# Optimization experiments

Measured on AMD Instinct MI355X. Metric: run time of the kernel, lower is better.

Reference implementation:

```python
import jax, jax.numpy as jnp
import numpy as np

B = 16384
N_NEIGH = 50
D = 64
NUM_USERS = 100000
NUM_ITEMS = 100000
NUM_ENTITIES = 200000


def setup_inputs() -> dict:
    key = jax.random.key(0)
    ks = jax.random.split(key, 16)
    s = 1.0 / np.sqrt(D)
    return {
        "user_indices": jax.random.randint(ks[0], (B,), 0, NUM_USERS),
        "item_indices": jax.random.randint(ks[1], (B,), 0, NUM_ITEMS),
        "kg_adj_batch": jax.random.randint(ks[2], (B, N_NEIGH), 0, NUM_ENTITIES),
        "user_table": jax.random.normal(ks[3], (NUM_USERS, D), jnp.float32),
        "item_table": jax.random.normal(ks[4], (NUM_ITEMS, D), jnp.float32),
        "entity_table": jax.random.normal(ks[5], (NUM_ENTITIES, D), jnp.float32),
        "attn_W": jax.random.normal(ks[6], (2 * D, 1), jnp.float32) * s,
        "attn_b": jnp.zeros((1,), jnp.float32),
        "kg_W1": jax.random.normal(ks[7], (D, D), jnp.float32) * s,
        "kg_b1": jnp.zeros((D,), jnp.float32),
        "kg_W2": jax.random.normal(ks[8], (D, D), jnp.float32) * s,
        "kg_b2": jnp.zeros((D,), jnp.float32),
        "comb_W": jax.random.normal(ks[9], (2 * D, D), jnp.float32) * s,
        "comb_b": jnp.zeros((D,), jnp.float32),
        "out_W": jax.random.normal(ks[10], (2 * D, 1), jnp.float32) * s,
        "out_b": jnp.zeros((1,), jnp.float32),
    }


def reference(user_indices, item_indices, kg_adj_batch,
              user_table, item_table, entity_table,
              attn_W, attn_b, kg_W1, kg_b1, kg_W2, kg_b2,
              comb_W, comb_b, out_W, out_b):
    user_emb = user_table[user_indices]          # [B, D]
    item_emb = item_table[item_indices]          # [B, D]
    nbr_idx = jnp.clip(kg_adj_batch, 0)
    neighbor_emb = entity_table[nbr_idx]         # [B, N, D]
    # attention_linear(cat([item, nbr])) == item @ Wi + nbr @ Wn + b (avoids [B,N,2D])
    Wi, Wn = attn_W[:D], attn_W[D:]
    attn_scores = item_emb @ Wi + jnp.einsum('bnd,do->bno', neighbor_emb, Wn)[..., 0] + attn_b  # [B, N]
    attn_scores = jax.nn.leaky_relu(attn_scores, negative_slope=0.2)
    attn_weights = jax.nn.softmax(attn_scores, axis=1)                 # softmax over neighbors
    neighbor_attn = jnp.einsum('bn,bnd->bd', attn_weights, neighbor_emb)
    refined_kg = jax.nn.relu(neighbor_attn @ kg_W1 + kg_b1) @ kg_W2 + kg_b2
    combined_item = jnp.concatenate([item_emb, refined_kg], axis=1)
    final_item_rep = jax.nn.relu(combined_item @ comb_W + comb_b)      # dropout = identity (eval)
    combined_user_item = jnp.concatenate([user_emb, final_item_rep], axis=1)
    score = (combined_user_item @ out_W + out_b)[:, 0]
    return score
```

## Files before the change

### kernel.cpp

```cpp
#include <hip/hip_runtime.h>

#define NN 50
#define D 64
#define GRP 10

typedef unsigned int uint32;
typedef unsigned short ushort16;

__device__ __forceinline__ float wave_sum64(float x) {
#pragma unroll
  for (int off = 32; off > 0; off >>= 1)
    x += __shfl_xor(x, off, 64);
  return x;
}

__device__ __forceinline__ float readlane_f(float v, int l) {
  return __uint_as_float(__builtin_amdgcn_readlane(__float_as_uint(v), l));
}

__device__ __forceinline__ ushort16 f32_to_bf16(float f) {
  uint32 u = __float_as_uint(f);
  u += 0x7FFF + ((u >> 16) & 1);
  return (ushort16)(u >> 16);
}

__global__ __launch_bounds__(256, 4) void kgat_prep(
    const float* __restrict__ ent_tab, const float* __restrict__ attn_W,
    float* __restrict__ proj, ushort16* __restrict__ ent_bf, int rows,
    int pblocks,
    const float* __restrict__ W2, const float* __restrict__ b2,
    const float* __restrict__ cW, const float* __restrict__ cb,
    float* __restrict__ W2cW, float* __restrict__ cb2)
{
  const int lane = threadIdx.x & 63;
  const int wv   = threadIdx.x >> 6;

  if ((int)blockIdx.x < pblocks) {
    const long wave = (long)blockIdx.x * 4 + wv;
    const long base = wave * GRP;
    if (base >= rows) return;
    const float Wn = attn_W[D + lane];
    float v[GRP];
#pragma unroll
    for (int i = 0; i < GRP; ++i) {
      long r = base + i; if (r > rows - 1) r = rows - 1;
      v[i] = ent_tab[r * D + lane];
    }
    float s[GRP];
#pragma unroll
    for (int i = 0; i < GRP; ++i)
      s[i] = wave_sum64(v[i] * Wn);
#pragma unroll
    for (int i = 0; i < GRP; ++i) {
      const long r = base + i;
      if (r < rows) ent_bf[r * D + lane] = f32_to_bf16(v[i]);
    }
    if (lane == 0) {
#pragma unroll
      for (int i = 0; i < GRP; ++i)
        if (base + i < rows) proj[base + i] = s[i];
    }
  } else {
    const int d = ((int)blockIdx.x - pblocks) * 4 + wv;
    float acc = 0.f;
#pragma unroll 8
    for (int k = 0; k < D; ++k)
      acc = fmaf(W2[d * D + k], cW[(D + k) * D + lane], acc);
    W2cW[d * D + lane] = acc;
    if (d == 0) {
      float a2 = 0.f;
#pragma unroll 8
      for (int k = 0; k < D; ++k)
        a2 = fmaf(b2[k], cW[(D + k) * D + lane], a2);
      cb2[lane] = cb[lane] + a2;
    }
  }
}

#define PGRP 5

__device__ __forceinline__ void load_pair_grp(uint32 (&buf)[PGRP],
                                              const int* __restrict__ adjb,
                                              const uint32* __restrict__ ent32,
                                              int g, int half, int sub) {
#pragma unroll
  for (int i = 0; i < PGRP; ++i) {
    const int p = g * PGRP + i;
    int t0 = adjb[2 * p + 0]; t0 = t0 < 0 ? 0 : t0;
    int t1 = adjb[2 * p + 1]; t1 = t1 < 0 ? 0 : t1;
    const int t = half ? t1 : t0;
    buf[i] = ent32[(size_t)t * 32 + sub];
  }
}

__device__ __forceinline__ void acc_pair_grp(const uint32 (&buf)[PGRP],
                                             float e, int g, int half,
                                             float& lo0, float& lo1,
                                             float& hi0, float& hi1) {
#pragma unroll
  for (int i = 0; i < PGRP; ++i) {
    const int p = g * PGRP + i;
    const float w0 = readlane_f(e, 2 * p + 0);
    const float w1 = readlane_f(e, 2 * p + 1);
    const float w  = half ? w1 : w0;
    const float lo = __uint_as_float(buf[i] << 16);
    const float hi = __uint_as_float(buf[i] & 0xFFFF0000u);
    if (i & 1) { lo1 = fmaf(w, lo, lo1); hi1 = fmaf(w, hi, hi1); }
    else       { lo0 = fmaf(w, lo, lo0); hi0 = fmaf(w, hi, hi0); }
  }
}

__global__ __launch_bounds__(256, 4) void kgat_attn2(
    const int* __restrict__ item_idx, const int* __restrict__ adj,
    const float* __restrict__ item_tab,
    const uint32* __restrict__ ent32, const float* __restrict__ proj,
    const float* __restrict__ attn_W, const float* __restrict__ attn_b,
    float* __restrict__ naws, int B)
{
  const int lane = threadIdx.x & 63;
  const int wv   = threadIdx.x >> 6;
  const int b    = blockIdx.x * 4 + wv;
  if (b >= B) return;
  const int half = lane >> 5;
  const int sub  = lane & 31;

  const int* adjb = adj + (long)b * NN;

  uint32 GA[PGRP], GB[PGRP];
  load_pair_grp(GA, adjb, ent32, 0, half, sub);
  load_pair_grp(GB, adjb, ent32, 1, half, sub);

  const float item = item_tab[(long)item_idx[b] * D + lane];
  const float base = wave_sum64(item * attn_W[lane]) + attn_b[0];

  const int myn = lane < NN ? lane : NN - 1;
  int mi = adjb[myn]; mi = mi < 0 ? 0 : mi;
  float s = proj[mi] + base;
  s = s > 0.f ? s : 0.2f * s;
  const float e = (lane < NN) ? __expf(s - 8.0f) : 0.f;
  const float denom = wave_sum64(e);

  float lo0 = 0.f, lo1 = 0.f, hi0 = 0.f, hi1 = 0.f;
  acc_pair_grp(GA, e, 0, half, lo0, lo1, hi0, hi1);
  load_pair_grp(GA, adjb, ent32, 2, half, sub);
  acc_pair_grp(GB, e, 1, half, lo0, lo1, hi0, hi1);
  load_pair_grp(GB, adjb, ent32, 3, half, sub);
  acc_pair_grp(GA, e, 2, half, lo0, lo1, hi0, hi1);
  load_pair_grp(GA, adjb, ent32, 4, half, sub);
  acc_pair_grp(GB, e, 3, half, lo0, lo1, hi0, hi1);
  acc_pair_grp(GA, e, 4, half, lo0, lo1, hi0, hi1);

  float nlo = lo0 + lo1;
  float nhi = hi0 + hi1;
  nlo += __shfl_xor(nlo, 32, 64);
  nhi += __shfl_xor(nhi, 32, 64);

  const float inv = 1.0f / denom;
  if (lane < 32) {
    float2 val = make_float2(nlo * inv, nhi * inv);
    *(float2*)(naws + (long)b * D + 2 * sub) = val;
  }
}

__global__ __launch_bounds__(256, 4) void kgat_mlpf(
    const int* __restrict__ user_idx, const int* __restrict__ item_idx,
    const float* __restrict__ user_tab, const float* __restrict__ item_tab,
    const float* __restrict__ naws,
    const float* __restrict__ W1, const float* __restrict__ b1,
    const float* __restrict__ cW,
    const float* __restrict__ W2cW, const float* __restrict__ cb2,
    const float* __restrict__ oW, const float* __restrict__ ob,
    float* __restrict__ out, int B)
{
  __shared__ __align__(16) float s_h[4 * 4 * D];

  const int lane = threadIdx.x & 63;
  const int wv   = threadIdx.x >> 6;
  const int b0   = (blockIdx.x * 4 + wv) * 4;
  if (b0 >= B) return;

  float* shA = s_h + (wv * 4 + 0) * D;
  float* shB = s_h + (wv * 4 + 1) * D;
  float* shC = s_h + (wv * 4 + 2) * D;
  float* shD = s_h + (wv * 4 + 3) * D;

  const int bA = b0 + 0 < B ? b0 + 0 : B - 1;
  const int bB = b0 + 1 < B ? b0 + 1 : B - 1;
  const int bC = b0 + 2 < B ? b0 + 2 : B - 1;
  const int bD = b0 + 3 < B ? b0 + 3 : B - 1;

  const int uA = __builtin_amdgcn_readfirstlane(bA);
  const int uB = __builtin_amdgcn_readfirstlane(bB);
  const int uC = __builtin_amdgcn_readfirstlane(bC);
  const int uD = __builtin_amdgcn_readfirstlane(bD);
  const float* napA = naws + (long)uA * D;
  const float* napB = naws + (long)uB * D;
  const float* napC = naws + (long)uC * D;
  const float* napD = naws + (long)uD * D;
  const int iiA = __builtin_amdgcn_readfirstlane(item_idx[bA]);
  const int iiB = __builtin_amdgcn_readfirstlane(item_idx[bB]);
  const int iiC = __builtin_amdgcn_readfirstlane(item_idx[bC]);
  const int iiD = __builtin_amdgcn_readfirstlane(item_idx[bD]);
  const float* itpA = item_tab + (long)iiA * D;
  const float* itpB = item_tab + (long)iiB * D;
  const float* itpC = item_tab + (long)iiC * D;
  const float* itpD = item_tab + (long)iiD * D;

  const float usA = user_tab[(long)user_idx[bA] * D + lane];
  const float usB = user_tab[(long)user_idx[bB] * D + lane];
  const float usC = user_tab[(long)user_idx[bC] * D + lane];
  const float usD = user_tab[(long)user_idx[bD] * D + lane];

  const float b1v  = b1[lane];
  const float cb2v = cb2[lane];
  float hA0 = b1v, hA1 = 0.f, hB0 = b1v, hB1 = 0.f;
  float hC0 = b1v, hC1 = 0.f, hD0 = b1v, hD1 = 0.f;
  float fA0 = cb2v, fA1 = 0.f, fB0 = cb2v, fB1 = 0.f;
  float fC0 = cb2v, fC1 = 0.f, fD0 = cb2v, fD1 = 0.f;
#pragma unroll
  for (int d = 0; d < D; d += 4) {
    const float v0 = W1[(d + 0) * D + lane];
    const float v1 = W1[(d + 1) * D + lane];
    const float v2 = W1[(d + 2) * D + lane];
    const float v3 = W1[(d + 3) * D + lane];
    const float w0 = cW[(d + 0) * D + lane];
    const float w1 = cW[(d + 1) * D + lane];
    const float w2 = cW[(d + 2) * D + lane];
    const float w3 = cW[(d + 3) * D + lane];
    const float4 aA = *(const float4*)(napA + d);
    const float4 aB = *(const float4*)(napB + d);
    const float4 aC = *(const float4*)(napC + d);
    const float4 aD = *(const float4*)(napD + d);
    const float4 iA = *(const float4*)(itpA + d);
    const float4 iB = *(const float4*)(itpB + d);
    const float4 iC = *(const float4*)(itpC + d);
    const float4 iD = *(const float4*)(itpD + d);
    hA0 = fmaf(aA.x, v0, hA0); hA1 = fmaf(aA.y, v1, hA1);
    hA0 = fmaf(aA.z, v2, hA0); hA1 = fmaf(aA.w, v3, hA1);
    hB0 = fmaf(aB.x, v0, hB0); hB1 = fmaf(aB.y, v1, hB1);
    hB0 = fmaf(aB.z, v2, hB0); hB1 = fmaf(aB.w, v3, hB1);
    hC0 = fmaf(aC.x, v0, hC0); hC1 = fmaf(aC.y, v1, hC1);
    hC0 = fmaf(aC.z, v2, hC0); hC1 = fmaf(aC.w, v3, hC1);
    hD0 = fmaf(aD.x, v0, hD0); hD1 = fmaf(aD.y, v1, hD1);
    hD0 = fmaf(aD.z, v2, hD0); hD1 = fmaf(aD.w, v3, hD1);
    fA0 = fmaf(iA.x, w0, fA0); fA1 = fmaf(iA.y, w1, fA1);
    fA0 = fmaf(iA.z, w2, fA0); fA1 = fmaf(iA.w, w3, fA1);
    fB0 = fmaf(iB.x, w0, fB0); fB1 = fmaf(iB.y, w1, fB1);
    fB0 = fmaf(iB.z, w2, fB0); fB1 = fmaf(iB.w, w3, fB1);
    fC0 = fmaf(iC.x, w0, fC0); fC1 = fmaf(iC.y, w1, fC1);
    fC0 = fmaf(iC.z, w2, fC0); fC1 = fmaf(iC.w, w3, fC1);
    fD0 = fmaf(iD.x, w0, fD0); fD1 = fmaf(iD.y, w1, fD1);
    fD0 = fmaf(iD.z, w2, fD0); fD1 = fmaf(iD.w, w3, fD1);
  }
  shA[lane] = fmaxf(hA0 + hA1, 0.f);
  shB[lane] = fmaxf(hB0 + hB1, 0.f);
  shC[lane] = fmaxf(hC0 + hC1, 0.f);
  shD[lane] = fmaxf(hD0 + hD1, 0.f);

#pragma unroll
  for (int d = 0; d < D; d += 4) {
    const float w0 = W2cW[(d + 0) * D + lane];
    const float w1 = W2cW[(d + 1) * D + lane];
    const float w2 = W2cW[(d + 2) * D + lane];
    const float w3 = W2cW[(d + 3) * D + lane];
    const float4 cA = *(const float4*)(shA + d);
    const float4 cB = *(const float4*)(shB + d);
    const float4 cC = *(const float4*)(shC + d);
    const float4 cD = *(const float4*)(shD + d);
    fA0 = fmaf(cA.x, w0, fA0); fA1 = fmaf(cA.y, w1, fA1);
    fA0 = fmaf(cA.z, w2, fA0); fA1 = fmaf(cA.w, w3, fA1);
    fB0 = fmaf(cB.x, w0, fB0); fB1 = fmaf(cB.y, w1, fB1);
    fB0 = fmaf(cB.z, w2, fB0); fB1 = fmaf(cB.w, w3, fB1);
    fC0 = fmaf(cC.x, w0, fC0); fC1 = fmaf(cC.y, w1, fC1);
    fC0 = fmaf(cC.z, w2, fC0); fC1 = fmaf(cC.w, w3, fC1);
    fD0 = fmaf(cD.x, w0, fD0); fD1 = fmaf(cD.y, w1, fD1);
    fD0 = fmaf(cD.z, w2, fD0); fD1 = fmaf(cD.w, w3, fD1);
  }
  const float fA = fmaxf(fA0 + fA1, 0.f);
  const float fB = fmaxf(fB0 + fB1, 0.f);
  const float fC = fmaxf(fC0 + fC1, 0.f);
  const float fD = fmaxf(fD0 + fD1, 0.f);

  const float oWu = oW[lane];
  const float oWf = oW[D + lane];
  const float ob0 = ob[0];
  const float scA = wave_sum64(fmaf(usA, oWu, fA * oWf));
  const float scB = wave_sum64(fmaf(usB, oWu, fB * oWf));
  const float scC = wave_sum64(fmaf(usC, oWu, fC * oWf));
  const float scD = wave_sum64(fmaf(usD, oWu, fD * oWf));
  if (lane == 0) {
    out[bA] = scA + ob0;
    if (bB != bA) out[bB] = scB + ob0;
    if (bC != bB) out[bC] = scC + ob0;
    if (bD != bC) out[bD] = scD + ob0;
  }
}

__device__ __forceinline__ void load_grp(float (&buf)[GRP],
                                         const int* __restrict__ adjb,
                                         const float* __restrict__ ent_tab,
                                         int g, int lane) {
#pragma unroll
  for (int i = 0; i < GRP; ++i) {
    int t = adjb[g * GRP + i];
    t = t < 0 ? 0 : t;
    buf[i] = ent_tab[(long)t * D + lane];
  }
}

__device__ __forceinline__ void proc_grp(const float (&buf)[GRP],
                                         float Wn, float base,
                                         float& l0, float& l1, float& na) {
  float ex[GRP];
#pragma unroll
  for (int i = 0; i < GRP; ++i) {
    float t = wave_sum64(buf[i] * Wn) + base;
    t = t > 0.f ? t : 0.2f * t;
    ex[i] = __expf(t - 8.0f);
  }
#pragma unroll
  for (int i = 0; i < GRP; ++i) {
    if (i & 1) l1 += ex[i]; else l0 += ex[i];
    na = fmaf(ex[i], buf[i], na);
  }
}

__global__ __launch_bounds__(256, 4) void kgat_r3(
    const int* __restrict__ user_idx, const int* __restrict__ item_idx,
    const int* __restrict__ adj,
    const float* __restrict__ user_tab, const float* __restrict__ item_tab,
    const float* __restrict__ ent_tab,
    const float* __restrict__ attn_W, const float* __restrict__ attn_b,
    const float* __restrict__ W1, const float* __restrict__ b1,
    const float* __restrict__ W2, const float* __restrict__ b2,
    const float* __restrict__ cW, const float* __restrict__ cb,
    const float* __restrict__ oW, const float* __restrict__ ob,
    float* __restrict__ out, int B)
{
  const int lane = threadIdx.x & 63;
  const int wv   = threadIdx.x >> 6;
  const int b    = blockIdx.x * 4 + wv;
  if (b >= B) return;

  const float user = user_tab[(long)user_idx[b] * D + lane];
  const float oWu  = oW[lane];
  const float oWf  = oW[D + lane];
  const float item = item_tab[(long)item_idx[b] * D + lane];
  const float Wi   = attn_W[lane];
  const float Wn   = attn_W[D + lane];
  const float base = wave_sum64(item * Wi) + attn_b[0];
  const int* adjb = adj + b * NN;

  float na = 0.f, l0 = 0.f, l1 = 0.f;
  float A[GRP], Bv[GRP];
  load_grp(A,  adjb, ent_tab, 0, lane);
  load_grp(Bv, adjb, ent_tab, 1, lane);
  proc_grp(A,  Wn, base, l0, l1, na);
  load_grp(A,  adjb, ent_tab, 2, lane);
  proc_grp(Bv, Wn, base, l0, l1, na);
  load_grp(Bv, adjb, ent_tab, 3, lane);
  proc_grp(A,  Wn, base, l0, l1, na);
  load_grp(A,  adjb, ent_tab, 4, lane);
  proc_grp(Bv, Wn, base, l0, l1, na);
  proc_grp(A,  Wn, base, l0, l1, na);
  na /= (l0 + l1);

  float h0 = b1[lane], h1 = 0.f, h2 = 0.f, h3 = 0.f;
#pragma unroll
  for (int d = 0; d < D; d += 4) {
    h0 = fmaf(readlane_f(na, d + 0), W1[(d + 0) * D + lane], h0);
    h1 = fmaf(readlane_f(na, d + 1), W1[(d + 1) * D + lane], h1);
    h2 = fmaf(readlane_f(na, d + 2), W1[(d + 2) * D + lane], h2);
    h3 = fmaf(readlane_f(na, d + 3), W1[(d + 3) * D + lane], h3);
  }
  const float h = fmaxf((h0 + h1) + (h2 + h3), 0.f);

  float r0 = b2[lane], r1 = 0.f, r2 = 0.f, r3 = 0.f;
#pragma unroll
  for (int d = 0; d < D; d += 4) {
    r0 = fmaf(readlane_f(h, d + 0), W2[(d + 0) * D + lane], r0);
    r1 = fmaf(readlane_f(h, d + 1), W2[(d + 1) * D + lane], r1);
    r2 = fmaf(readlane_f(h, d + 2), W2[(d + 2) * D + lane], r2);
    r3 = fmaf(readlane_f(h, d + 3), W2[(d + 3) * D + lane], r3);
  }
  const float r = (r0 + r1) + (r2 + r3);

  float f0 = cb[lane], f1 = 0.f, f2 = 0.f, f3 = 0.f;
#pragma unroll
  for (int k = 0; k < D; k += 4) {
    f0 = fmaf(readlane_f(item, k + 0), cW[(k + 0) * D + lane], f0);
    f1 = fmaf(readlane_f(item, k + 1), cW[(k + 1) * D + lane], f1);
    f2 = fmaf(readlane_f(item, k + 2), cW[(k + 2) * D + lane], f2);
    f3 = fmaf(readlane_f(item, k + 3), cW[(k + 3) * D + lane], f3);
  }
#pragma unroll
  for (int k = 0; k < D; k += 4) {
    f0 = fmaf(readlane_f(r, k + 0), cW[(D + k + 0) * D + lane], f0);
    f1 = fmaf(readlane_f(r, k + 1), cW[(D + k + 1) * D + lane], f1);
    f2 = fmaf(readlane_f(r, k + 2), cW[(D + k + 2) * D + lane], f2);
    f3 = fmaf(readlane_f(r, k + 3), cW[(D + k + 3) * D + lane], f3);
  }
  const float f = fmaxf((f0 + f1) + (f2 + f3), 0.f);

  const float sc = wave_sum64(fmaf(user, oWu, f * oWf));
  if (lane == 0) out[b] = sc + ob[0];
}

extern "C" void kernel_launch(void* const* d_in, const int* in_sizes, int n_in,
                              void* d_out, int out_size, void* d_ws, size_t ws_size,
                              hipStream_t stream) {
  const int*   user_idx = (const int*)d_in[0];
  const int*   item_idx = (const int*)d_in[1];
  const int*   adj      = (const int*)d_in[2];
  const float* user_tab = (const float*)d_in[3];
  const float* item_tab = (const float*)d_in[4];
  const float* ent_tab  = (const float*)d_in[5];
  const float* attn_W   = (const float*)d_in[6];
  const float* attn_b   = (const float*)d_in[7];
  const float* W1       = (const float*)d_in[8];
  const float* b1       = (const float*)d_in[9];
  const float* W2       = (const float*)d_in[10];
  const float* b2       = (const float*)d_in[11];
  const float* cW       = (const float*)d_in[12];
  const float* cb       = (const float*)d_in[13];
  const float* oW       = (const float*)d_in[14];
  const float* ob       = (const float*)d_in[15];
  float* out = (float*)d_out;

  const int B    = in_sizes[0];
  const int rows = in_sizes[5] / D;

  const size_t off_bf = ((size_t)rows * 4 + 255) & ~(size_t)255;
  const size_t off_na = (off_bf + (size_t)rows * D * 2 + 255) & ~(size_t)255;
  const size_t off_w2 = (off_na + (size_t)B * D * 4 + 255) & ~(size_t)255;
  const size_t off_cb = off_w2 + (size_t)D * D * 4;
  const size_t need   = off_cb + (size_t)D * 4;

  if (ws_size >= need) {
    float*    proj   = (float*)d_ws;
    ushort16* ent_bf = (ushort16*)((char*)d_ws + off_bf);
    float*    naws   = (float*)((char*)d_ws + off_na);
    float*    W2cW   = (float*)((char*)d_ws + off_w2);
    float*    cb2    = (float*)((char*)d_ws + off_cb);
    const int waves   = (rows + GRP - 1) / GRP;
    const int pblocks = (waves + 3) / 4;
    const int ablocks = (B + 3) / 4;
    const int mblocks = (B + 15) / 16;
    kgat_prep<<<pblocks + 16, 256, 0, stream>>>(ent_tab, attn_W, proj, ent_bf,
                                                rows, pblocks, W2, b2, cW, cb,
                                                W2cW, cb2);
    kgat_attn2<<<ablocks, 256, 0, stream>>>(item_idx, adj, item_tab,
                                            (const uint32*)ent_bf, proj,
                                            attn_W, attn_b, naws, B);
    kgat_mlpf<<<mblocks, 256, 0, stream>>>(user_idx, item_idx, user_tab,
                                           item_tab, naws, W1, b1, cW,
                                           W2cW, cb2, oW, ob, out, B);
  } else {
    const int blocks = (B + 3) / 4;
    kgat_r3<<<blocks, 256, 0, stream>>>(user_idx, item_idx, adj,
                                        user_tab, item_tab, ent_tab,
                                        attn_W, attn_b, W1, b1, W2, b2,
                                        cW, cb, oW, ob, out, B);
  }
}
```

Before: 51.74 us.

## Move first KG MLP layer into attention kernel and fuse second-stage matmuls

```diff
diff --git a/kernel.cpp b/kernel.cpp
--- a/kernel.cpp
+++ b/kernel.cpp
@@ -110,12 +110,13 @@
   }
 }
 
-__global__ __launch_bounds__(256, 4) void kgat_attn2(
+__global__ __launch_bounds__(256, 4) void kgat_attn2h(
     const int* __restrict__ item_idx, const int* __restrict__ adj,
     const float* __restrict__ item_tab,
     const uint32* __restrict__ ent32, const float* __restrict__ proj,
     const float* __restrict__ attn_W, const float* __restrict__ attn_b,
-    float* __restrict__ naws, int B)
+    const float* __restrict__ W1, const float* __restrict__ b1,
+    float* __restrict__ hws, int B)
 {
   const int lane = threadIdx.x & 63;
   const int wv   = threadIdx.x >> 6;
@@ -154,36 +155,34 @@
   float nhi = hi0 + hi1;
   nlo += __shfl_xor(nlo, 32, 64);
   nhi += __shfl_xor(nhi, 32, 64);
-
   const float inv = 1.0f / denom;
-  if (lane < 32) {
-    float2 val = make_float2(nlo * inv, nhi * inv);
-    *(float2*)(naws + (long)b * D + 2 * sub) = val;
-  }
-}
-
-__global__ __launch_bounds__(256, 4) void kgat_mlpf(
+
+  float h0 = 0.f, h1 = 0.f;
+#pragma unroll
+  for (int k = 0; k < D; k += 2) {
+    const float a0 = readlane_f(nlo, k >> 1);
+    const float a1 = readlane_f(nhi, k >> 1);
+    h0 = fmaf(a0, W1[(k + 0) * D + lane], h0);
+    h1 = fmaf(a1, W1[(k + 1) * D + lane], h1);
+  }
+  const float h = fmaxf(fmaf(h0 + h1, inv, b1[lane]), 0.f);
+  hws[(long)b * D + lane] = h;
+}
+
+__global__ __launch_bounds__(256, 4) void kgat_mlp2u(
     const int* __restrict__ user_idx, const int* __restrict__ item_idx,
     const float* __restrict__ user_tab, const float* __restrict__ item_tab,
-    const float* __restrict__ naws,
-    const float* __restrict__ W1, const float* __restrict__ b1,
+    const float* __restrict__ hws,
     const float* __restrict__ cW,
     const float* __restrict__ W2cW, const float* __restrict__ cb2,
     const float* __restrict__ oW, const float* __restrict__ ob,
     float* __restrict__ out, int B)
 {
-  __shared__ __align__(16) float s_h[4 * 4 * D];
-
   const int lane = threadIdx.x & 63;
   const int wv   = threadIdx.x >> 6;
   const int b0   = (blockIdx.x * 4 + wv) * 4;
   if (b0 >= B) return;
 
-  float* shA = s_h + (wv * 4 + 0) * D;
-  float* shB = s_h + (wv * 4 + 1) * D;
-  float* shC = s_h + (wv * 4 + 2) * D;
-  float* shD = s_h + (wv * 4 + 3) * D;
-
   const int bA = b0 + 0 < B ? b0 + 0 : B - 1;
   const int bB = b0 + 1 < B ? b0 + 1 : B - 1;
   const int bC = b0 + 2 < B ? b0 + 2 : B - 1;
@@ -193,10 +192,10 @@
   const int uB = __builtin_amdgcn_readfirstlane(bB);
   const int uC = __builtin_amdgcn_readfirstlane(bC);
   const int uD = __builtin_amdgcn_readfirstlane(bD);
-  const float* napA = naws + (long)uA * D;
-  const float* napB = naws + (long)uB * D;
-  const float* napC = naws + (long)uC * D;
-  const float* napD = naws + (long)uD * D;
+  const float* hpA = hws + (long)uA * D;
+  const float* hpB = hws + (long)uB * D;
+  const float* hpC = hws + (long)uC * D;
+  const float* hpD = hws + (long)uD * D;
   const int iiA = __builtin_amdgcn_readfirstlane(item_idx[bA]);
   const int iiB = __builtin_amdgcn_readfirstlane(item_idx[bB]);
   const int iiC = __builtin_amdgcn_readfirstlane(item_idx[bC]);
@@ -211,70 +210,43 @@
   const float usC = user_tab[(long)user_idx[bC] * D + lane];
   const float usD = user_tab[(long)user_idx[bD] * D + lane];
 
-  const float b1v  = b1[lane];
   const float cb2v = cb2[lane];
-  float hA0 = b1v, hA1 = 0.f, hB0 = b1v, hB1 = 0.f;
-  float hC0 = b1v, hC1 = 0.f, hD0 = b1v, hD1 = 0.f;
   float fA0 = cb2v, fA1 = 0.f, fB0 = cb2v, fB1 = 0.f;
   float fC0 = cb2v, fC1 = 0.f, fD0 = cb2v, fD1 = 0.f;
 #pragma unroll
   for (int d = 0; d < D; d += 4) {
-    const float v0 = W1[(d + 0) * D + lane];
-    const float v1 = W1[(d + 1) * D + lane];
-    const float v2 = W1[(d + 2) * D + lane];
-    const float v3 = W1[(d + 3) * D + lane];
     const float w0 = cW[(d + 0) * D + lane];
     const float w1 = cW[(d + 1) * D + lane];
     const float w2 = cW[(d + 2) * D + lane];
     const float w3 = cW[(d + 3) * D + lane];
-    const float4 aA = *(const float4*)(napA + d);
-    const float4 aB = *(const float4*)(napB + d);
-    const float4 aC = *(const float4*)(napC + d);
-    const float4 aD = *(const float4*)(napD + d);
+    const float v0 = W2cW[(d + 0) * D + lane];
+    const float v1 = W2cW[(d + 1) * D + lane];
+    const float v2 = W2cW[(d + 2) * D + lane];
+    const float v3 = W2cW[(d + 3) * D + lane];
     const float4 iA = *(const float4*)(itpA + d);
     const float4 iB = *(const float4*)(itpB + d);
     const float4 iC = *(const float4*)(itpC + d);
     const float4 iD = *(const float4*)(itpD + d);
-    hA0 = fmaf(aA.x, v0, hA0); hA1 = fmaf(aA.y, v1, hA1);
-    hA0 = fmaf(aA.z, v2, hA0); hA1 = fmaf(aA.w, v3, hA1);
-    hB0 = fmaf(aB.x, v0, hB0); hB1 = fmaf(aB.y, v1, hB1);
-    hB0 = fmaf(aB.z, v2, hB0); hB1 = fmaf(aB.w, v3, hB1);
-    hC0 = fmaf(aC.x, v0, hC0); hC1 = fmaf(aC.y, v1, hC1);
-    hC0 = fmaf(aC.z, v2, hC0); hC1 = fmaf(aC.w, v3, hC1);
-    hD0 = fmaf(aD.x, v0, hD0); hD1 = fmaf(aD.y, v1, hD1);
-    hD0 = fmaf(aD.z, v2, hD0); hD1 = fmaf(aD.w, v3, hD1);
+    const float4 hA = *(const float4*)(hpA + d);
+    const float4 hB = *(const float4*)(hpB + d);
+    const float4 hC = *(const float4*)(hpC + d);
+    const float4 hD = *(const float4*)(hpD + d);
     fA0 = fmaf(iA.x, w0, fA0); fA1 = fmaf(iA.y, w1, fA1);
     fA0 = fmaf(iA.z, w2, fA0); fA1 = fmaf(iA.w, w3, fA1);
+    fA0 = fmaf(hA.x, v0, fA0); fA1 = fmaf(hA.y, v1, fA1);
+    fA0 = fmaf(hA.z, v2, fA0); fA1 = fmaf(hA.w, v3, fA1);
     fB0 = fmaf(iB.x, w0, fB0); fB1 = fmaf(iB.y, w1, fB1);
     fB0 = fmaf(iB.z, w2, fB0); fB1 = fmaf(iB.w, w3, fB1);
+    fB0 = fmaf(hB.x, v0, fB0); fB1 = fmaf(hB.y, v1, fB1);
+    fB0 = fmaf(hB.z, v2, fB0); fB1 = fmaf(hB.w, v3, fB1);
     fC0 = fmaf(iC.x, w0, fC0); fC1 = fmaf(iC.y, w1, fC1);
     fC0 = fmaf(iC.z, w2, fC0); fC1 = fmaf(iC.w, w3, fC1);
+    fC0 = fmaf(hC.x, v0, fC0); fC1 = fmaf(hC.y, v1, fC1);
+    fC0 = fmaf(hC.z, v2, fC0); fC1 = fmaf(hC.w, v3, fC1);
     fD0 = fmaf(iD.x, w0, fD0); fD1 = fmaf(iD.y, w1, fD1);
     fD0 = fmaf(iD.z, w2, fD0); fD1 = fmaf(iD.w, w3, fD1);
-  }
-  shA[lane] = fmaxf(hA0 + hA1, 0.f);
-  shB[lane] = fmaxf(hB0 + hB1, 0.f);
-  shC[lane] = fmaxf(hC0 + hC1, 0.f);
-  shD[lane] = fmaxf(hD0 + hD1, 0.f);
-
-#pragma unroll
-  for (int d = 0; d < D; d += 4) {
-    const float w0 = W2cW[(d + 0) * D + lane];
-    const float w1 = W2cW[(d + 1) * D + lane];
-    const float w2 = W2cW[(d + 2) * D + lane];
-    const float w3 = W2cW[(d + 3) * D + lane];
-    const float4 cA = *(const float4*)(shA + d);
-    const float4 cB = *(const float4*)(shB + d);
-    const float4 cC = *(const float4*)(shC + d);
-    const float4 cD = *(const float4*)(shD + d);
-    fA0 = fmaf(cA.x, w0, fA0); fA1 = fmaf(cA.y, w1, fA1);
-    fA0 = fmaf(cA.z, w2, fA0); fA1 = fmaf(cA.w, w3, fA1);
-    fB0 = fmaf(cB.x, w0, fB0); fB1 = fmaf(cB.y, w1, fB1);
-    fB0 = fmaf(cB.z, w2, fB0); fB1 = fmaf(cB.w, w3, fB1);
-    fC0 = fmaf(cC.x, w0, fC0); fC1 = fmaf(cC.y, w1, fC1);
-    fC0 = fmaf(cC.z, w2, fC0); fC1 = fmaf(cC.w, w3, fC1);
-    fD0 = fmaf(cD.x, w0, fD0); fD1 = fmaf(cD.y, w1, fD1);
-    fD0 = fmaf(cD.z, w2, fD0); fD1 = fmaf(cD.w, w3, fD1);
+    fD0 = fmaf(hD.x, v0, fD0); fD1 = fmaf(hD.y, v1, fD1);
+    fD0 = fmaf(hD.z, v2, fD0); fD1 = fmaf(hD.w, v3, fD1);
   }
   const float fA = fmaxf(fA0 + fA1, 0.f);
   const float fB = fmaxf(fB0 + fB1, 0.f);
@@ -431,15 +403,15 @@
   const int rows = in_sizes[5] / D;
 
   const size_t off_bf = ((size_t)rows * 4 + 255) & ~(size_t)255;
-  const size_t off_na = (off_bf + (size_t)rows * D * 2 + 255) & ~(size_t)255;
-  const size_t off_w2 = (off_na + (size_t)B * D * 4 + 255) & ~(size_t)255;
+  const size_t off_h  = (off_bf + (size_t)rows * D * 2 + 255) & ~(size_t)255;
+  const size_t off_w2 = (off_h + (size_t)B * D * 4 + 255) & ~(size_t)255;
   const size_t off_cb = off_w2 + (size_t)D * D * 4;
   const size_t need   = off_cb + (size_t)D * 4;
 
   if (ws_size >= need) {
     float*    proj   = (float*)d_ws;
     ushort16* ent_bf = (ushort16*)((char*)d_ws + off_bf);
-    float*    naws   = (float*)((char*)d_ws + off_na);
+    float*    hws    = (float*)((char*)d_ws + off_h);
     float*    W2cW   = (float*)((char*)d_ws + off_w2);
     float*    cb2    = (float*)((char*)d_ws + off_cb);
     const int waves   = (rows + GRP - 1) / GRP;
@@ -449,12 +421,12 @@
     kgat_prep<<<pblocks + 16, 256, 0, stream>>>(ent_tab, attn_W, proj, ent_bf,
                                                 rows, pblocks, W2, b2, cW, cb,
                                                 W2cW, cb2);
-    kgat_attn2<<<ablocks, 256, 0, stream>>>(item_idx, adj, item_tab,
-                                            (const uint32*)ent_bf, proj,
-                                            attn_W, attn_b, naws, B);
-    kgat_mlpf<<<mblocks, 256, 0, stream>>>(user_idx, item_idx, user_tab,
-                                           item_tab, naws, W1, b1, cW,
-                                           W2cW, cb2, oW, ob, out, B);
+    kgat_attn2h<<<ablocks, 256, 0, stream>>>(item_idx, adj, item_tab,
+                                             (const uint32*)ent_bf, proj,
+                                             attn_W, attn_b, W1, b1, hws, B);
+    kgat_mlp2u<<<mblocks, 256, 0, stream>>>(user_idx, item_idx, user_tab,
+                                            item_tab, hws, cW, W2cW, cb2,
+                                            oW, ob, out, B);
   } else {
     const int blocks = (B + 3) / 4;
     kgat_r3<<<blocks, 256, 0, stream>>>(user_idx, item_idx, adj,
```

After: 56.85 us. 9.9% more time.
